# Kernel optimization log

Hardware: AMD Instinct MI355X
Metric: run time of the kernel (lower is better)

## Reference

```python
import jax, jax.numpy as jnp
import numpy as np

N_HEAD = 16
BLOCK = 128  # segment length sl=128, dilation ratio dr=1 (hardcoded in forward)


def setup_inputs() -> dict:
    key = jax.random.key(0)
    k1, k2, k3 = jax.random.split(key, 3)
    B, T, C = 4, 8192, 2048
    x = jax.random.normal(k1, (B, T, C), dtype=jnp.float32)
    W_qkv = jax.random.normal(k2, (C, 3 * C), dtype=jnp.float32) * 0.02
    W_proj = jax.random.normal(k3, (C, C), dtype=jnp.float32) * 0.02
    return {"x": x, "W_qkv": W_qkv, "W_proj": W_proj}


def reference(x, W_qkv, W_proj):
    B, T, C = x.shape
    H = N_HEAD
    dh = C // H
    nb = T // BLOCK  # number of 128-token segments

    qkv = x @ W_qkv                      # (B, T, 3C)
    q, k, v = jnp.split(qkv, 3, axis=-1)

    def to_blocks(t):
        # (B, T, C) -> (B, nb, H, BLOCK, dh)
        return t.reshape(B, nb, BLOCK, H, dh).transpose(0, 1, 3, 2, 4)

    q, k, v = to_blocks(q), to_blocks(k), to_blocks(v)

    scale = 1.0 / jnp.sqrt(jnp.asarray(dh, dtype=x.dtype))
    scores = jnp.einsum('bnhqd,bnhkd->bnhqk', q, k) * scale  # (B, nb, H, BLOCK, BLOCK)
    causal = jnp.tril(jnp.ones((BLOCK, BLOCK), dtype=bool))
    scores = jnp.where(causal, scores, -jnp.inf)
    att = jax.nn.softmax(scores, axis=-1)
    out = jnp.einsum('bnhqk,bnhkd->bnhqd', att, v)
    # Single (sl, dr) branch => lse-weighted scattering collapses to weight 1.
    y = out.transpose(0, 1, 3, 2, 4).reshape(B, T, C)
    return y @ W_proj
```

## Files before the change

kernel.cpp:

```cpp
#include <hip/hip_runtime.h>

typedef unsigned short u16;
typedef unsigned int u32;
typedef __bf16 bf16x8 __attribute__((ext_vector_type(8)));
typedef float f32x4 __attribute__((ext_vector_type(4)));

#define DIM_M 32768
#define DIM_C 2048
#define DIM_3C 6144
#define N_HEAD 16
#define DH 128

__device__ __forceinline__ u16 f2bf(float f) {
  u32 x = __float_as_uint(f);
  u32 r = x + 0x7fffu + ((x >> 16) & 1u);
  return (u16)(r >> 16);
}

__device__ __forceinline__ void async_copy16(const void* g, void* l) {
  __builtin_amdgcn_global_load_lds((const __attribute__((address_space(1))) u32*)g,
                                   (__attribute__((address_space(3))) u32*)l,
                                   16, 0, 0);
}

__global__ __launch_bounds__(256) void cvt_f32_bf16(const float* __restrict__ in,
                                                    u16* __restrict__ out) {
  size_t i = ((size_t)blockIdx.x * 256 + threadIdx.x) * 4;
  float4 v = *(const float4*)(in + i);
  union { u16 s[4]; uint2 u; } o;
  o.s[0] = f2bf(v.x); o.s[1] = f2bf(v.y); o.s[2] = f2bf(v.z); o.s[3] = f2bf(v.w);
  *(uint2*)(out + i) = o.u;
}

__global__ __launch_bounds__(256) void transpose_cvt(const float* __restrict__ W,
                                                     u16* __restrict__ Wt,
                                                     int K, int N) {
  __shared__ u16 t[32][33];
  int nb = blockIdx.x * 32, kb = blockIdx.y * 32;
  int r = threadIdx.x >> 5, c = threadIdx.x & 31;
#pragma unroll
  for (int i = 0; i < 4; ++i) {
    int rr = i * 8 + r;
    t[rr][c] = f2bf(W[(size_t)(kb + rr) * N + nb + c]);
  }
  __syncthreads();
#pragma unroll
  for (int i = 0; i < 4; ++i) {
    int rr = i * 8 + r;
    Wt[(size_t)(nb + rr) * K + kb + c] = t[c][rr];
  }
}

template <bool OUT_BF16>
__global__ __launch_bounds__(256) void gemm_bt(const u16* __restrict__ A,
                                               const u16* __restrict__ Bt,
                                               void* __restrict__ Cv,
                                               int M, int N, int K) {
  __shared__ u16 As[128 * 32];
  __shared__ u16 Bs[128 * 32];
  const int tid = threadIdx.x;
  const int wave = tid >> 6;
  const int lane = tid & 63;
  const int ln15 = lane & 15;
  const int quad = lane >> 4;
  const int srow = lane >> 2;
  const int scol = (lane & 3) * 8;
  const int rowblk = blockIdx.y * 128;
  const int colblk = blockIdx.x * 128;
  const int wr = (wave >> 1) * 64;
  const int wc = (wave & 1) * 64;

  f32x4 acc[4][4] = {};

  const int ch0 = wave, ch1 = wave + 4;
  const u16* ga0 = A + (size_t)(rowblk + ch0 * 16 + srow) * K + scol;
  const u16* ga1 = A + (size_t)(rowblk + ch1 * 16 + srow) * K + scol;
  const u16* gb0 = Bt + (size_t)(colblk + ch0 * 16 + srow) * K + scol;
  const u16* gb1 = Bt + (size_t)(colblk + ch1 * 16 + srow) * K + scol;

  for (int kt = 0; kt < K; kt += 32) {
    __syncthreads();
    async_copy16(ga0 + kt, &As[ch0 * 512]);
    async_copy16(ga1 + kt, &As[ch1 * 512]);
    async_copy16(gb0 + kt, &Bs[ch0 * 512]);
    async_copy16(gb1 + kt, &Bs[ch1 * 512]);
    __syncthreads();
    bf16x8 a[4], b[4];
#pragma unroll
    for (int i = 0; i < 4; ++i)
      a[i] = *(const bf16x8*)&As[(wr + i * 16 + ln15) * 32 + quad * 8];
#pragma unroll
    for (int j = 0; j < 4; ++j)
      b[j] = *(const bf16x8*)&Bs[(wc + j * 16 + ln15) * 32 + quad * 8];
#pragma unroll
    for (int i = 0; i < 4; ++i)
#pragma unroll
      for (int j = 0; j < 4; ++j)
        acc[i][j] = __builtin_amdgcn_mfma_f32_16x16x32_bf16(a[i], b[j], acc[i][j], 0, 0, 0);
  }

#pragma unroll
  for (int i = 0; i < 4; ++i) {
#pragma unroll
    for (int j = 0; j < 4; ++j) {
      const float* ap = (const float*)&acc[i][j];
#pragma unroll
      for (int r = 0; r < 4; ++r) {
        int row = rowblk + wr + i * 16 + quad * 4 + r;
        int col = colblk + wc + j * 16 + ln15;
        if (OUT_BF16)
          ((u16*)Cv)[(size_t)row * N + col] = f2bf(ap[r]);
        else
          ((float*)Cv)[(size_t)row * N + col] = ap[r];
      }
    }
  }
}

__global__ __launch_bounds__(256) void attn_block(const u16* __restrict__ qkv,
                                                  u16* __restrict__ y) {
  __shared__ u16 buf0[128 * 128];
  __shared__ u16 buf1[128 * 128];
  const int h = blockIdx.x, n = blockIdx.y, b = blockIdx.z;
  const size_t rowbase = ((size_t)b * 8192 + (size_t)n * 128) * DIM_3C;
  const int qcol = h * DH, kcol = DIM_C + h * DH, vcol = 2 * DIM_C + h * DH;
  const int tid = threadIdx.x;
  const int wave = tid >> 6, lane = tid & 63;
  const int ln15 = lane & 15, quad = lane >> 4;
  const int r0 = wave * 32;

#pragma unroll
  for (int it = 0; it < 16; ++it) {
    int f = tid + it * 256;
    int tk = f >> 5;
    int dg = f & 31;
    int off = tk * 128 + (((dg >> 1) ^ (tk & 15)) * 8) + (dg & 1) * 4;
    uint2 qv = *(const uint2*)(qkv + rowbase + (size_t)tk * DIM_3C + qcol + dg * 4);
    *(uint2*)(buf0 + off) = qv;
    uint2 kv = *(const uint2*)(qkv + rowbase + (size_t)tk * DIM_3C + kcol + dg * 4);
    *(uint2*)(buf1 + off) = kv;
  }
  __syncthreads();

  f32x4 acc[2][8] = {};
#pragma unroll
  for (int ks = 0; ks < 4; ++ks) {
    bf16x8 aq[2], bk[8];
#pragma unroll
    for (int i = 0; i < 2; ++i) {
      int row = r0 + i * 16 + ln15;
      aq[i] = *(const bf16x8*)(buf0 + row * 128 + (((ks * 4 + quad) ^ (row & 15)) * 8));
    }
#pragma unroll
    for (int j = 0; j < 8; ++j) {
      int row = j * 16 + ln15;
      bk[j] = *(const bf16x8*)(buf1 + row * 128 + (((ks * 4 + quad) ^ (row & 15)) * 8));
    }
#pragma unroll
    for (int i = 0; i < 2; ++i)
#pragma unroll
      for (int j = 0; j < 8; ++j)
        acc[i][j] = __builtin_amdgcn_mfma_f32_16x16x32_bf16(aq[i], bk[j], acc[i][j], 0, 0, 0);
  }

  const float scale = 0.08838834764831845f;
  float lrow[2][4];
#pragma unroll
  for (int i = 0; i < 2; ++i) {
#pragma unroll
    for (int r = 0; r < 4; ++r) {
      int row = r0 + i * 16 + quad * 4 + r;
      float m = -1e30f;
#pragma unroll
      for (int j = 0; j < 8; ++j) {
        float* ap = (float*)&acc[i][j];
        int col = j * 16 + ln15;
        float s = ap[r] * scale;
        if (col > row) s = -1e30f;
        ap[r] = s;
        m = fmaxf(m, s);
      }
#pragma unroll
      for (int off = 1; off < 16; off <<= 1) m = fmaxf(m, __shfl_xor(m, off));
      float l = 0.f;
#pragma unroll
      for (int j = 0; j < 8; ++j) {
        float* ap = (float*)&acc[i][j];
        float p = __expf(ap[r] - m);
        ap[r] = p;
        l += p;
      }
#pragma unroll
      for (int off = 1; off < 16; off <<= 1) l += __shfl_xor(l, off);
      lrow[i][r] = l;
    }
  }
  __syncthreads();

#pragma unroll
  for (int i = 0; i < 2; ++i)
#pragma unroll
    for (int j = 0; j < 8; ++j) {
      const float* ap = (const float*)&acc[i][j];
#pragma unroll
      for (int r = 0; r < 4; ++r) {
        int row = r0 + i * 16 + quad * 4 + r;
        int col = j * 16 + ln15;
        buf0[row * 128 + (((col >> 3) ^ (row & 15)) * 8) + (col & 7)] = f2bf(ap[r]);
      }
    }
#pragma unroll
  for (int it = 0; it < 16; ++it) {
    int f = tid + it * 256;
    int tk = f >> 5;
    int dg = f & 31;
    uint2 vv = *(const uint2*)(qkv + rowbase + (size_t)tk * DIM_3C + vcol + dg * 4);
    union { u16 s[4]; uint2 u; } tmp;
    tmp.u = vv;
#pragma unroll
    for (int j = 0; j < 4; ++j) {
      int dd = dg * 4 + j;
      buf1[dd * 128 + (((tk >> 3) ^ (dd & 15)) * 8) + (tk & 7)] = tmp.s[j];
    }
  }
  __syncthreads();

  f32x4 accO[2][8] = {};
#pragma unroll
  for (int ks = 0; ks < 4; ++ks) {
    bf16x8 ap[2], bv[8];
#pragma unroll
    for (int i = 0; i < 2; ++i) {
      int row = r0 + i * 16 + ln15;
      ap[i] = *(const bf16x8*)(buf0 + row * 128 + (((ks * 4 + quad) ^ (row & 15)) * 8));
    }
#pragma unroll
    for (int j = 0; j < 8; ++j) {
      int row = j * 16 + ln15;
      bv[j] = *(const bf16x8*)(buf1 + row * 128 + (((ks * 4 + quad) ^ (row & 15)) * 8));
    }
#pragma unroll
    for (int i = 0; i < 2; ++i)
#pragma unroll
      for (int j = 0; j < 8; ++j)
        accO[i][j] = __builtin_amdgcn_mfma_f32_16x16x32_bf16(ap[i], bv[j], accO[i][j], 0, 0, 0);
  }

  u16* yb = y + ((size_t)b * 8192 + (size_t)n * 128) * DIM_C + h * DH;
#pragma unroll
  for (int i = 0; i < 2; ++i)
#pragma unroll
    for (int j = 0; j < 8; ++j) {
      const float* op = (const float*)&accO[i][j];
#pragma unroll
      for (int r = 0; r < 4; ++r) {
        int row = r0 + i * 16 + quad * 4 + r;
        int col = j * 16 + ln15;
        yb[(size_t)row * DIM_C + col] = f2bf(op[r] / lrow[i][r]);
      }
    }
}

extern "C" void kernel_launch(void* const* d_in, const int* in_sizes, int n_in,
                              void* d_out, int out_size, void* d_ws, size_t ws_size,
                              hipStream_t stream) {
  const float* x = (const float*)d_in[0];
  const float* W_qkv = (const float*)d_in[1];
  const float* W_proj = (const float*)d_in[2];
  float* out = (float*)d_out;

  char* ws = (char*)d_ws;
  u16* xb = (u16*)ws;
  u16* yb = xb;
  u16* qkvb = (u16*)(ws + (size_t)134217728);
  u16* Wqt = (u16*)(ws + (size_t)134217728 + 402653184);
  u16* Wpt = Wqt + (size_t)6144 * 2048;

  cvt_f32_bf16<<<dim3(65536), dim3(256), 0, stream>>>(x, xb);
  transpose_cvt<<<dim3(DIM_3C / 32, DIM_C / 32), dim3(256), 0, stream>>>(W_qkv, Wqt, DIM_C, DIM_3C);
  transpose_cvt<<<dim3(DIM_C / 32, DIM_C / 32), dim3(256), 0, stream>>>(W_proj, Wpt, DIM_C, DIM_C);
  gemm_bt<true><<<dim3(DIM_3C / 128, DIM_M / 128), dim3(256), 0, stream>>>(
      xb, Wqt, (void*)qkvb, DIM_M, DIM_3C, DIM_C);
  attn_block<<<dim3(N_HEAD, 64, 4), dim3(256), 0, stream>>>(qkvb, yb);
  gemm_bt<false><<<dim3(DIM_C / 128, DIM_M / 128), dim3(256), 0, stream>>>(
      yb, Wpt, (void*)out, DIM_M, DIM_C, DIM_C);
}
```

Before: 2.001 ms.

## Replace GEMM with 256x256 double-buffered, swizzled, phase-scheduled MFMA kernel

Both GEMMs move from a 128x128, single-buffered, K=32 tile kernel to a 512-thread kernel with 256x256 tiles and K=64 steps. Shared-memory loads are double-buffered and XOR-swizzled to avoid bank conflicts. Workgroup IDs are remapped across the 8 XCDs to improve L2 locality. Each K-step is split into barrier-separated load and MFMA phases with setprio, so async copies overlap with matrix math. The cost is much higher LDS use (128KB per block) and register pressure, which limits occupancy and risks spills.

```diff
diff --git a/kernel.cpp b/kernel.cpp
--- a/kernel.cpp
+++ b/kernel.cpp
@@ -21,6 +21,14 @@
   __builtin_amdgcn_global_load_lds((const __attribute__((address_space(1))) u32*)g,
                                    (__attribute__((address_space(3))) u32*)l,
                                    16, 0, 0);
+}
+
+__device__ __forceinline__ void phase_bar() {
+  asm volatile("" ::: "memory");
+  __builtin_amdgcn_sched_barrier(0);
+  __builtin_amdgcn_s_barrier();
+  __builtin_amdgcn_sched_barrier(0);
+  asm volatile("" ::: "memory");
 }
 
 __global__ __launch_bounds__(256) void cvt_f32_bf16(const float* __restrict__ in,
@@ -51,63 +59,116 @@
   }
 }
 
+#define STAGE(OP, BUF, KOFF)                                                        \
+  do {                                                                              \
+    _Pragma("unroll") for (int l_ = 0; l_ < 4; ++l_)                                \
+        async_copy16(g##OP + (size_t)l_ * 64 * K + (KOFF),                          \
+                     &s##OP[BUF][(l_ * 8 + w) * 512]);                              \
+  } while (0)
+
+#define LDA_Q(QA)                                                                   \
+  do {                                                                              \
+    _Pragma("unroll") for (int f_ = 0; f_ < 4; ++f_)                                \
+        _Pragma("unroll") for (int ks_ = 0; ks_ < 2; ++ks_) {                       \
+      int r_ = WR + (QA) * 64 + f_ * 16 + ln15;                                     \
+      a[f_][ks_] = *(const bf16x8*)&sAc[r_ * 64 + (((ks_ * 4 + quad) ^ (r_ & 7)) * 8)]; \
+    }                                                                               \
+  } while (0)
+
+#define LDB_Q(QB)                                                                   \
+  do {                                                                              \
+    _Pragma("unroll") for (int f_ = 0; f_ < 2; ++f_)                                \
+        _Pragma("unroll") for (int ks_ = 0; ks_ < 2; ++ks_) {                       \
+      int r_ = WC + (QB) * 32 + f_ * 16 + ln15;                                     \
+      b[f_][ks_] = *(const bf16x8*)&sBc[r_ * 64 + (((ks_ * 4 + quad) ^ (r_ & 7)) * 8)]; \
+    }                                                                               \
+  } while (0)
+
+#define MMA_Q(QA, QB)                                                               \
+  do {                                                                              \
+    __builtin_amdgcn_s_setprio(1);                                                  \
+    _Pragma("unroll") for (int ks_ = 0; ks_ < 2; ++ks_)                             \
+        _Pragma("unroll") for (int f_ = 0; f_ < 4; ++f_)                            \
+            _Pragma("unroll") for (int g_ = 0; g_ < 2; ++g_)                        \
+                acc[(QA) * 4 + f_][(QB) * 2 + g_] =                                 \
+        __builtin_amdgcn_mfma_f32_16x16x32_bf16(                                    \
+            a[f_][ks_], b[g_][ks_], acc[(QA) * 4 + f_][(QB) * 2 + g_], 0, 0, 0);    \
+    __builtin_amdgcn_s_setprio(0);                                                  \
+  } while (0)
+
 template <bool OUT_BF16>
-__global__ __launch_bounds__(256) void gemm_bt(const u16* __restrict__ A,
-                                               const u16* __restrict__ Bt,
-                                               void* __restrict__ Cv,
-                                               int M, int N, int K) {
-  __shared__ u16 As[128 * 32];
-  __shared__ u16 Bs[128 * 32];
+__global__ __launch_bounds__(512, 2) void gemm256(const u16* __restrict__ A,
+                                                  const u16* __restrict__ Bt,
+                                                  void* __restrict__ Cv,
+                                                  int M, int N, int K) {
+  __shared__ u16 sA[2][256 * 64];
+  __shared__ u16 sB[2][256 * 64];
+
+  const int NT = N >> 8;
+  int wg = blockIdx.x;
+  {
+    const int cpx = gridDim.x >> 3;
+    wg = (wg & 7) * cpx + (wg >> 3);
+  }
+  const int rowblk = (wg / NT) << 8;
+  const int colblk = (wg % NT) << 8;
+
   const int tid = threadIdx.x;
-  const int wave = tid >> 6;
-  const int lane = tid & 63;
-  const int ln15 = lane & 15;
-  const int quad = lane >> 4;
-  const int srow = lane >> 2;
-  const int scol = (lane & 3) * 8;
-  const int rowblk = blockIdx.y * 128;
-  const int colblk = blockIdx.x * 128;
-  const int wr = (wave >> 1) * 64;
-  const int wc = (wave & 1) * 64;
-
-  f32x4 acc[4][4] = {};
-
-  const int ch0 = wave, ch1 = wave + 4;
-  const u16* ga0 = A + (size_t)(rowblk + ch0 * 16 + srow) * K + scol;
-  const u16* ga1 = A + (size_t)(rowblk + ch1 * 16 + srow) * K + scol;
-  const u16* gb0 = Bt + (size_t)(colblk + ch0 * 16 + srow) * K + scol;
-  const u16* gb1 = Bt + (size_t)(colblk + ch1 * 16 + srow) * K + scol;
-
-  for (int kt = 0; kt < K; kt += 32) {
+  const int w = tid >> 6, lane = tid & 63;
+  const int ln15 = lane & 15, quad = lane >> 4;
+  const int WR = (w >> 2) << 7;
+  const int WC = (w & 3) << 6;
+
+  const int srow = (w << 3) + (lane >> 3);
+  const int scl = (lane & 7) ^ ((lane >> 3) & 7);
+  const u16* gA = A + (size_t)(rowblk + srow) * K + scl * 8;
+  const u16* gB = Bt + (size_t)(colblk + srow) * K + scl * 8;
+
+  f32x4 acc[8][4] = {};
+  bf16x8 a[4][2], b[2][2];
+  const int KT = K >> 6;
+
+  STAGE(A, 0, 0);
+  STAGE(B, 0, 0);
+  __syncthreads();
+
+  for (int kt = 0; kt < KT; ++kt) {
+    const int cur = kt & 1, nxt = cur ^ 1;
+    const u16* sAc = sA[cur];
+    const u16* sBc = sB[cur];
+    const size_t gk = (size_t)(kt + 1) * 64;
+    const bool pf = (kt + 1) < KT;
+
+    if (pf) STAGE(A, nxt, gk);
+    LDA_Q(0);
+    LDB_Q(0);
+    phase_bar();
+    MMA_Q(0, 0);
+    phase_bar();
+    if (pf) STAGE(B, nxt, gk);
+    LDB_Q(1);
+    phase_bar();
+    MMA_Q(0, 1);
+    phase_bar();
+    LDA_Q(1);
+    phase_bar();
+    MMA_Q(1, 1);
+    phase_bar();
+    LDB_Q(0);
+    phase_bar();
+    MMA_Q(1, 0);
     __syncthreads();
-    async_copy16(ga0 + kt, &As[ch0 * 512]);
-    async_copy16(ga1 + kt, &As[ch1 * 512]);
-    async_copy16(gb0 + kt, &Bs[ch0 * 512]);
-    async_copy16(gb1 + kt, &Bs[ch1 * 512]);
-    __syncthreads();
-    bf16x8 a[4], b[4];
-#pragma unroll
-    for (int i = 0; i < 4; ++i)
-      a[i] = *(const bf16x8*)&As[(wr + i * 16 + ln15) * 32 + quad * 8];
-#pragma unroll
-    for (int j = 0; j < 4; ++j)
-      b[j] = *(const bf16x8*)&Bs[(wc + j * 16 + ln15) * 32 + quad * 8];
-#pragma unroll
-    for (int i = 0; i < 4; ++i)
-#pragma unroll
-      for (int j = 0; j < 4; ++j)
-        acc[i][j] = __builtin_amdgcn_mfma_f32_16x16x32_bf16(a[i], b[j], acc[i][j], 0, 0, 0);
-  }
-
-#pragma unroll
-  for (int i = 0; i < 4; ++i) {
-#pragma unroll
-    for (int j = 0; j < 4; ++j) {
-      const float* ap = (const float*)&acc[i][j];
+  }
+
+#pragma unroll
+  for (int fi = 0; fi < 8; ++fi) {
+#pragma unroll
+    for (int fj = 0; fj < 4; ++fj) {
+      const float* ap = (const float*)&acc[fi][fj];
 #pragma unroll
       for (int r = 0; r < 4; ++r) {
-        int row = rowblk + wr + i * 16 + quad * 4 + r;
-        int col = colblk + wc + j * 16 + ln15;
+        int row = rowblk + WR + fi * 16 + quad * 4 + r;
+        int col = colblk + WC + fj * 16 + ln15;
         if (OUT_BF16)
           ((u16*)Cv)[(size_t)row * N + col] = f2bf(ap[r]);
         else
@@ -279,9 +340,9 @@
   cvt_f32_bf16<<<dim3(65536), dim3(256), 0, stream>>>(x, xb);
   transpose_cvt<<<dim3(DIM_3C / 32, DIM_C / 32), dim3(256), 0, stream>>>(W_qkv, Wqt, DIM_C, DIM_3C);
   transpose_cvt<<<dim3(DIM_C / 32, DIM_C / 32), dim3(256), 0, stream>>>(W_proj, Wpt, DIM_C, DIM_C);
-  gemm_bt<true><<<dim3(DIM_3C / 128, DIM_M / 128), dim3(256), 0, stream>>>(
+  gemm256<true><<<dim3((DIM_M / 256) * (DIM_3C / 256)), dim3(512), 0, stream>>>(
       xb, Wqt, (void*)qkvb, DIM_M, DIM_3C, DIM_C);
   attn_block<<<dim3(N_HEAD, 64, 4), dim3(256), 0, stream>>>(qkvb, yb);
-  gemm_bt<false><<<dim3(DIM_C / 128, DIM_M / 128), dim3(256), 0, stream>>>(
+  gemm256<false><<<dim3((DIM_M / 256) * (DIM_C / 256)), dim3(512), 0, stream>>>(
       yb, Wpt, (void*)out, DIM_M, DIM_C, DIM_C);
 }
```

Result: slower. 2.066 ms (+3.2%).
